# Optimization experiments

Hardware: AMD Instinct MI355X
Metric: run time of the kernel (lower is better)

Reference implementation:

```python
import jax, jax.numpy as jnp
import numpy as np

B, E, D, NH, NP = 4, 32, 1024, 16, 4
LQ = E * E
DH = D // NH


def layer_norm(x, g, b, eps=1e-6):
    m = x.mean(-1, keepdims=True)
    v = ((x - m) ** 2).mean(-1, keepdims=True)
    return (x - m) / jnp.sqrt(v + eps) * g + b


def get_ref(H, W):
    # matches MSCrossAttnBlock.get_reference_points: centers normalized to [0,1], (x, y) order
    ys, xs = jnp.meshgrid((jnp.arange(H, dtype=jnp.float32) + 0.5) / H,
                          (jnp.arange(W, dtype=jnp.float32) + 0.5) / W, indexing='ij')
    return jnp.stack([xs.ravel(), ys.ravel()], -1)  # (H*W, 2)


def bilinear_sample(value_l, loc, H, W):
    # value_l: (N, nH, H*W, dh); loc: (N, Lq, nH, P, 2) normalized to [0,1]
    # replicates F.grid_sample(align_corners=False, padding_mode='zeros') with grid = 2*loc - 1
    N, Lq, nH, P, _ = loc.shape
    x = loc[..., 0] * W - 0.5
    y = loc[..., 1] * H - 0.5
    x0 = jnp.floor(x)
    y0 = jnp.floor(y)
    wx1 = x - x0
    wy1 = y - y0
    out = 0.0
    for dy, wy in ((0, 1.0 - wy1), (1, wy1)):
        for dx, wx in ((0, 1.0 - wx1), (1, wx1)):
            xi = x0 + dx
            yi = y0 + dy
            valid = (xi >= 0) & (xi < W) & (yi >= 0) & (yi < H)
            idx = (jnp.clip(yi, 0, H - 1) * W + jnp.clip(xi, 0, W - 1)).astype(jnp.int32)
            idx_t = idx.transpose(0, 2, 1, 3).reshape(N, nH, Lq * P)  # (N, nH, Lq*P)
            g = jnp.take_along_axis(value_l, idx_t[..., None], axis=2)  # (N, nH, Lq*P, dh)
            g = g.reshape(N, nH, Lq, P, -1).transpose(0, 2, 1, 3, 4)  # (N, Lq, nH, P, dh)
            w = (wx * wy) * valid.astype(value_l.dtype)
            out = out + g * w[..., None]
    return out


def msdeform(query, ref, inp, shapes, Wv, bv, Wo, bo, Wa, ba, Wp, bp):
    # MSDeformAttn forward (no padding mask)
    N, Lq, d = query.shape
    nL = len(shapes)
    value = (inp @ Wv.T + bv).reshape(N, -1, NH, DH).transpose(0, 2, 1, 3)  # (N, nH, Lin, dh)
    off = (query @ Wo.T + bo).reshape(N, Lq, NH, nL, NP, 2)
    attw = jax.nn.softmax((query @ Wa.T + ba).reshape(N, Lq, NH, nL * NP), axis=-1)
    attw = attw.reshape(N, Lq, NH, nL, NP)
    normalizer = jnp.array([[w, h] for (h, w) in shapes], dtype=query.dtype)  # (nL, 2) = [W, H]
    loc = ref[None, :, None, None, None, :] + off / normalizer[None, None, None, :, None, :]
    out = 0.0
    start = 0
    for l, (H, W) in enumerate(shapes):
        sampled = bilinear_sample(value[:, :, start:start + H * W], loc[:, :, :, l], H, W)
        out = out + (sampled * attw[:, :, :, l, :, None]).sum(3)  # (N, Lq, nH, dh)
        start += H * W
    return out.reshape(N, Lq, d) @ Wp.T + bp


def setup_inputs() -> dict:
    key = jax.random.key(0)
    ks = iter(jax.random.split(key, 64))
    def rnd(shape, scale):
        return jax.random.normal(next(ks), shape, dtype=jnp.float32) * scale
    inp = {}
    for i in range(4):
        inp[f'src{i}'] = rnd((B, LQ, D), 1.0)
    for nm in ('qn', 'fn', 'n1'):
        inp[nm + '_g'] = jnp.ones((D,), jnp.float32)
        inp[nm + '_b'] = jnp.zeros((D,), jnp.float32)
    inp['gamma1'] = rnd((D,), 0.1)
    inp['gamma2'] = rnd((D,), 0.1)
    ws = D ** -0.5
    for pre, nl in (('ca', 4), ('sa', 1)):
        inp[pre + '_vw'] = rnd((D, D), ws)
        inp[pre + '_vb'] = jnp.zeros((D,), jnp.float32)
        inp[pre + '_ow'] = rnd((NH * nl * NP * 2, D), ws)
        inp[pre + '_ob'] = rnd((NH * nl * NP * 2,), 0.1)
        inp[pre + '_aw'] = rnd((NH * nl * NP, D), ws)
        inp[pre + '_ab'] = jnp.zeros((NH * nl * NP,), jnp.float32)
        inp[pre + '_pw'] = rnd((D, D), ws)
        inp[pre + '_pb'] = jnp.zeros((D,), jnp.float32)
    return inp


def reference(src0, src1, src2, src3, qn_g, qn_b, fn_g, fn_b, n1_g, n1_b, gamma1, gamma2,
              ca_vw, ca_vb, ca_ow, ca_ob, ca_aw, ca_ab, ca_pw, ca_pb,
              sa_vw, sa_vb, sa_ow, sa_ob, sa_aw, sa_ab, sa_pw, sa_pb):
    shapes4 = [(E, E)] * 4
    feat = jnp.concatenate([src0, src1, src2, src3], axis=1)  # (B, 4*LQ, D)
    query = src3  # srcs[-1], pos embed is None
    ref = get_ref(E, E)  # (LQ, 2)
    attn = msdeform(layer_norm(query, qn_g, qn_b), ref, layer_norm(feat, fn_g, fn_b),
                    shapes4, ca_vw, ca_vb, ca_ow, ca_ob, ca_aw, ca_ab, ca_pw, ca_pb)
    attn1 = layer_norm(attn, n1_g, n1_b)
    attn2 = msdeform(attn1, ref, attn1, [(E, E)],
                     sa_vw, sa_vb, sa_ow, sa_ob, sa_aw, sa_ab, sa_pw, sa_pb)
    attn = attn + gamma2 * attn2
    return query + gamma1 * attn
```

## Files before the change

kernel.cpp:

```cpp
#include <hip/hip_runtime.h>


#define DEV __device__ __forceinline__

typedef float f32x4 __attribute__((ext_vector_type(4)));
typedef __bf16 bf16x8 __attribute__((ext_vector_type(8)));

DEV unsigned short f2bf(float f) {
  union { float f; unsigned u; } a; a.f = f;
  unsigned r = a.u + 0x7fffu + ((a.u >> 16) & 1u);
  return (unsigned short)(r >> 16);
}
DEV float bf2f(unsigned short h) {
  union { unsigned u; float f; } a; a.u = ((unsigned)h) << 16;
  return a.f;
}

struct CvtArgs {
  const float* src[8];
  unsigned short* dst;
  int off4[9];
};
struct LnArgs {
  const float* s[4];
  const float* fg; const float* fb; const float* qg; const float* qb;
  unsigned short* f_out; unsigned short* q_out;
};

DEV void ln_row_wave(const float* __restrict__ xr, const float* __restrict__ g,
                     const float* __restrict__ b,
                     unsigned short* __restrict__ op_row) {
  const int lane = threadIdx.x & 63;
  float4 v[4];
  float s = 0.f, s2 = 0.f;
  #pragma unroll
  for (int j = 0; j < 4; ++j) {
    v[j] = ((const float4*)xr)[lane + 64 * j];
    s  += v[j].x + v[j].y + v[j].z + v[j].w;
    s2 += v[j].x*v[j].x + v[j].y*v[j].y + v[j].z*v[j].z + v[j].w*v[j].w;
  }
  #pragma unroll
  for (int o = 32; o; o >>= 1) { s += __shfl_xor(s, o); s2 += __shfl_xor(s2, o); }
  const float mean = s * (1.f / 1024.f);
  const float rstd = rsqrtf(s2 * (1.f / 1024.f) - mean * mean + 1e-6f);
  #pragma unroll
  for (int j = 0; j < 4; ++j) {
    float4 gg = ((const float4*)g)[lane + 64 * j];
    float4 bb = ((const float4*)b)[lane + 64 * j];
    ushort4 r;
    r.x = f2bf((v[j].x - mean) * rstd * gg.x + bb.x);
    r.y = f2bf((v[j].y - mean) * rstd * gg.y + bb.y);
    r.z = f2bf((v[j].z - mean) * rstd * gg.z + bb.z);
    r.w = f2bf((v[j].w - mean) * rstd * gg.w + bb.w);
    ((ushort4*)op_row)[lane + 64 * j] = r;
  }
}

__global__ __launch_bounds__(256) void prep_kernel(CvtArgs a, LnArgs L) {
  if (blockIdx.x < 5056) {
    int i = blockIdx.x * 256 + threadIdx.x;
    int seg = 0;
    #pragma unroll
    for (int s = 1; s < 8; ++s) seg += (i >= a.off4[s]) ? 1 : 0;
    const float4 v = ((const float4*)a.src[seg])[i - a.off4[seg]];
    unsigned short* o = a.dst + (size_t)i * 4;
    o[0] = f2bf(v.x); o[1] = f2bf(v.y); o[2] = f2bf(v.z); o[3] = f2bf(v.w);
  } else {
    int row = (blockIdx.x - 5056) * 4 + (threadIdx.x >> 6);
    if (row < 16384) {
      int l = row >> 12, inner = row & 4095;
      int orow = (inner >> 10) * 4096 + l * 1024 + (inner & 1023);
      ln_row_wave(L.s[l] + (size_t)inner * 1024, L.fg, L.fb,
                  L.f_out + (size_t)orow * 1024);
    } else {
      int inner = row - 16384;
      ln_row_wave(L.s[3] + (size_t)inner * 1024, L.qg, L.qb,
                  L.q_out + (size_t)inner * 1024);
    }
  }
}

__global__ __launch_bounds__(256) void ln_wave_kernel(
    const float* __restrict__ x, const float* __restrict__ g,
    const float* __restrict__ b, unsigned short* __restrict__ out) {
  int row = blockIdx.x * 4 + (threadIdx.x >> 6);
  ln_row_wave(x + (size_t)row * 1024, g, b, out + (size_t)row * 1024);
}

struct GemmP {
  const unsigned short* A; const unsigned short* W;
  void* C; void* C1; void* C2;
  const float* b0; const float* b1; const float* b2;
  const float* src3; const float* g1; const float* g2; const float* attnp;
  int M, N, K, tilesM;
};

template <int BM, int BN, int EPI>
DEV void gemm_body(const GemmP& P, int id, unsigned short* sA,
                   unsigned short* sB) {
  constexpr int WMT = BM / 2, WNT = BN / 2;
  constexpr int MF = WMT / 16, NF = WNT / 16;
  constexpr int PA = BM / 64, PB = BN / 64;
  const int tid = threadIdx.x;
  const int wave = tid >> 6, lane = tid & 63;
  const int wm = (wave & 1) * WMT, wn = (wave >> 1) * WNT;
  const int m0 = (id % P.tilesM) * BM;
  const int n0 = (id / P.tilesM) * BN;
  const int lq = lane >> 4, lm = lane & 15;
  const int r16 = lane >> 2;
  const int cst = lane & 3;
  const int csrc = cst ^ ((r16 >> 1) & 3);
  const int aslot = lq ^ ((lm >> 1) & 3);

  f32x4 acc[MF][NF] = {};
  bf16x8 ald[2][PA], bld[2][PB];

  #pragma unroll 1
  for (int k0 = 0; k0 < P.K; k0 += 64) {
    #pragma unroll
    for (int s = 0; s < 2; ++s) {
      #pragma unroll
      for (int p = 0; p < PA; ++p) {
        int grow = m0 + (wave + 4 * p) * 16 + r16;
        ald[s][p] = *(const bf16x8*)(P.A + (size_t)grow * P.K + k0 + s * 32 + csrc * 8);
      }
      #pragma unroll
      for (int p = 0; p < PB; ++p) {
        int grow = min(n0 + (wave + 4 * p) * 16 + r16, P.N - 1);
        bld[s][p] = *(const bf16x8*)(P.W + (size_t)grow * P.K + k0 + s * 32 + csrc * 8);
      }
    }
    __syncthreads();
    #pragma unroll
    for (int s = 0; s < 2; ++s) {
      #pragma unroll
      for (int p = 0; p < PA; ++p)
        *(bf16x8*)(sA + s * BM * 32 + (wave + 4 * p) * 512 + (r16 * 4 + cst) * 8) = ald[s][p];
      #pragma unroll
      for (int p = 0; p < PB; ++p)
        *(bf16x8*)(sB + s * BN * 32 + (wave + 4 * p) * 512 + (r16 * 4 + cst) * 8) = bld[s][p];
    }
    __syncthreads();
    #pragma unroll
    for (int s = 0; s < 2; ++s) {
      bf16x8 af[MF], bfr[NF];
      #pragma unroll
      for (int mi = 0; mi < MF; ++mi)
        af[mi] = *(const bf16x8*)(sA + s * BM * 32 + ((wm >> 4) + mi) * 512 + lm * 32 + aslot * 8);
      #pragma unroll
      for (int ni = 0; ni < NF; ++ni)
        bfr[ni] = *(const bf16x8*)(sB + s * BN * 32 + ((wn >> 4) + ni) * 512 + lm * 32 + aslot * 8);
      #pragma unroll
      for (int mi = 0; mi < MF; ++mi)
        #pragma unroll
        for (int ni = 0; ni < NF; ++ni)
          acc[mi][ni] = __builtin_amdgcn_mfma_f32_16x16x32_bf16(
              af[mi], bfr[ni], acc[mi][ni], 0, 0, 0);
    }
  }

  #pragma unroll
  for (int mi = 0; mi < MF; ++mi) {
    #pragma unroll
    for (int ni = 0; ni < NF; ++ni) {
      const int col = n0 + wn + ni * 16 + lm;
      #pragma unroll
      for (int r2 = 0; r2 < 4; ++r2) {
        const int row = m0 + wm + mi * 16 + lq * 4 + r2;
        float v = acc[mi][ni][r2];
        if constexpr (EPI == 0) {
          ((float*)P.C)[(size_t)row * 1024 + col] = v + P.b0[col];
        } else if constexpr (EPI == 1) {
          ((unsigned short*)P.C)[(size_t)row * 1024 + col] = f2bf(v + P.b0[col]);
        } else if constexpr (EPI == 2) {
          if (col < 512)
            ((float*)P.C)[(size_t)row * 512 + col] = v + P.b0[col];
          else
            ((float*)P.C1)[(size_t)row * 256 + col - 512] = v + P.b1[col - 512];
        } else if constexpr (EPI == 3) {
          if (col < 1024)
            ((unsigned short*)P.C)[(size_t)row * 1024 + col] = f2bf(v + P.b0[col]);
          else if (col < 1152)
            ((float*)P.C1)[(size_t)row * 128 + col - 1024] = v + P.b1[col - 1024];
          else if (col < 1216)
            ((float*)P.C2)[(size_t)row * 64 + col - 1152] = v + P.b2[col - 1152];
        } else {
          size_t i = (size_t)row * 1024 + col;
          float vv = v + P.b0[col];
          ((float*)P.C)[i] = P.src3[i] + P.g1[col] * (P.attnp[i] + P.g2[col] * vv);
        }
      }
    }
  }
}

template <int BM, int BN, int EPI>
__global__ __launch_bounds__(256) void gemm_v3(GemmP P) {
  extern __shared__ __align__(16) unsigned short smem[];
  gemm_body<BM, BN, EPI>(P, blockIdx.x, smem, smem + BM * 64);
}

template <int BM, int BN>
__global__ __launch_bounds__(256) void gemm_dual(GemmP Pv, GemmP Po, int split) {
  extern __shared__ __align__(16) unsigned short smem[];
  if ((int)blockIdx.x < split)
    gemm_body<BM, BN, 1>(Pv, blockIdx.x, smem, smem + BM * 64);
  else
    gemm_body<BM, BN, 2>(Po, blockIdx.x - split, smem, smem + BM * 64);
}

template <int NLEV>
__global__ __launch_bounds__(256) void ms_sample_fused(
    const unsigned short* __restrict__ value, const float* __restrict__ off,
    const float* __restrict__ logits, unsigned short* __restrict__ out) {
  const int nq = blockIdx.x;
  const int wave = threadIdx.x >> 6, lane = threadIdx.x & 63;
  const int h = (wave << 2) + (lane >> 4);
  const int c = (lane & 15) << 2;
  const int q = nq & 1023, n = nq >> 10;
  const float* offp = off + ((size_t)nq * 16 + h) * (NLEV * 8);
  const float* lgp  = logits + ((size_t)nq * 16 + h) * (NLEV * 4);

  float lg[NLEV * 4];
  #pragma unroll
  for (int i = 0; i < NLEV; ++i) {
    float4 v = ((const float4*)lgp)[i];
    lg[4*i] = v.x; lg[4*i+1] = v.y; lg[4*i+2] = v.z; lg[4*i+3] = v.w;
  }
  float mx = lg[0];
  #pragma unroll
  for (int i = 1; i < NLEV * 4; ++i) mx = fmaxf(mx, lg[i]);
  float ssum = 0.f;
  #pragma unroll
  for (int i = 0; i < NLEV * 4; ++i) { lg[i] = __expf(lg[i] - mx); ssum += lg[i]; }
  const float inv = 1.f / ssum;

  const float fqx = (float)(q & 31), fqy = (float)(q >> 5);
  float a0 = 0.f, a1 = 0.f, a2 = 0.f, a3 = 0.f;

  #pragma unroll
  for (int l = 0; l < NLEV; ++l) {
    const unsigned short* vl =
        value + ((size_t)(n * NLEV + l) << 20) + h * 64 + c;
    #pragma unroll
    for (int p = 0; p < 4; ++p) {
      float2 o2 = ((const float2*)offp)[l * 4 + p];
      float aw = lg[l * 4 + p] * inv;
      float xx = fqx + o2.x, yy = fqy + o2.y;
      float xf = floorf(xx), yf = floorf(yy);
      float fx = xx - xf, fy = yy - yf;
      int ix = (int)xf, iy = (int)yf;
      int ix1 = ix + 1, iy1 = iy + 1;
      float vx0 = ((unsigned)ix  < 32u) ? 1.f : 0.f;
      float vx1 = ((unsigned)ix1 < 32u) ? 1.f : 0.f;
      float vy0 = ((unsigned)iy  < 32u) ? 1.f : 0.f;
      float vy1 = ((unsigned)iy1 < 32u) ? 1.f : 0.f;
      int cx0 = min(max(ix, 0), 31), cx1 = min(max(ix1, 0), 31);
      int cy0 = min(max(iy, 0), 31), cy1 = min(max(iy1, 0), 31);
      float w00 = (1.f - fx) * (1.f - fy) * vx0 * vy0 * aw;
      float w01 = fx * (1.f - fy) * vx1 * vy0 * aw;
      float w10 = (1.f - fx) * fy * vx0 * vy1 * aw;
      float w11 = fx * fy * vx1 * vy1 * aw;
      ushort4 u00 = *(const ushort4*)(vl + ((size_t)(cy0 * 32 + cx0) << 10));
      ushort4 u01 = *(const ushort4*)(vl + ((size_t)(cy0 * 32 + cx1) << 10));
      ushort4 u10 = *(const ushort4*)(vl + ((size_t)(cy1 * 32 + cx0) << 10));
      ushort4 u11 = *(const ushort4*)(vl + ((size_t)(cy1 * 32 + cx1) << 10));
      a0 += w00 * bf2f(u00.x) + w01 * bf2f(u01.x) + w10 * bf2f(u10.x) + w11 * bf2f(u11.x);
      a1 += w00 * bf2f(u00.y) + w01 * bf2f(u01.y) + w10 * bf2f(u10.y) + w11 * bf2f(u11.y);
      a2 += w00 * bf2f(u00.z) + w01 * bf2f(u01.z) + w10 * bf2f(u10.z) + w11 * bf2f(u11.z);
      a3 += w00 * bf2f(u00.w) + w01 * bf2f(u01.w) + w10 * bf2f(u10.w) + w11 * bf2f(u11.w);
    }
  }
  ushort4 r;
  r.x = f2bf(a0); r.y = f2bf(a1); r.z = f2bf(a2); r.w = f2bf(a3);
  *(ushort4*)(out + ((size_t)nq * 16 + h) * 64 + c) = r;
}

extern "C" void kernel_launch(void* const* d_in, const int* in_sizes, int n_in,
                              void* d_out, int out_size, void* d_ws,
                              size_t ws_size, hipStream_t stream) {
  (void)in_sizes; (void)n_in; (void)out_size; (void)ws_size;
  const float* src[4] = {(const float*)d_in[0], (const float*)d_in[1],
                         (const float*)d_in[2], (const float*)d_in[3]};
  const float* qn_g = (const float*)d_in[4];
  const float* qn_b = (const float*)d_in[5];
  const float* fn_g = (const float*)d_in[6];
  const float* fn_b = (const float*)d_in[7];
  const float* n1_g = (const float*)d_in[8];
  const float* n1_b = (const float*)d_in[9];
  const float* gamma1 = (const float*)d_in[10];
  const float* gamma2 = (const float*)d_in[11];
  const float* ca_vw = (const float*)d_in[12];
  const float* ca_vb = (const float*)d_in[13];
  const float* ca_ow = (const float*)d_in[14];
  const float* ca_ob = (const float*)d_in[15];
  const float* ca_aw = (const float*)d_in[16];
  const float* ca_ab = (const float*)d_in[17];
  const float* ca_pw = (const float*)d_in[18];
  const float* ca_pb = (const float*)d_in[19];
  const float* sa_vw = (const float*)d_in[20];
  const float* sa_vb = (const float*)d_in[21];
  const float* sa_ow = (const float*)d_in[22];
  const float* sa_ob = (const float*)d_in[23];
  const float* sa_aw = (const float*)d_in[24];
  const float* sa_ab = (const float*)d_in[25];
  const float* sa_pw = (const float*)d_in[26];
  const float* sa_pb = (const float*)d_in[27];

  char* wsp = (char*)d_ws;
  size_t off = 0;
  auto alloc = [&](size_t bytes) {
    char* r = wsp + off;
    off = (off + bytes + 255) & ~(size_t)255;
    return r;
  };
  const size_t MB = 1024 * 1024;
  unsigned short* w_ca_vw = (unsigned short*)alloc(1024 * 1024 * 2);
  unsigned short* w_ca_ow = (unsigned short*)alloc(512 * 1024 * 2);
  unsigned short* w_ca_aw = (unsigned short*)alloc(256 * 1024 * 2);
  unsigned short* w_ca_pw = (unsigned short*)alloc(1024 * 1024 * 2);
  unsigned short* w_sa_vw = (unsigned short*)alloc(1024 * 1024 * 2);
  unsigned short* w_sa_ow = (unsigned short*)alloc(128 * 1024 * 2);
  unsigned short* w_sa_aw = (unsigned short*)alloc(64 * 1024 * 2);
  unsigned short* w_sa_pw = (unsigned short*)alloc(1024 * 1024 * 2);
  (void)w_ca_aw; (void)w_sa_ow; (void)w_sa_aw;
  char* R1 = alloc(32 * MB);
  char* R2 = alloc(32 * MB);
  char* R3 = alloc(8 * MB);
  char* R4 = alloc(8 * MB);
  char* R5 = alloc(4 * MB);

  unsigned short* f_ln    = (unsigned short*)R1;
  float*          attn    = (float*)R1;
  unsigned short* attn1   = (unsigned short*)(R1 + 16 * MB);
  unsigned short* samp_sa = (unsigned short*)(R1 + 24 * MB);
  unsigned short* val_ca  = (unsigned short*)R2;
  unsigned short* val_sa  = (unsigned short*)R2;
  unsigned short* q_ln    = (unsigned short*)R3;
  unsigned short* samp_ca = (unsigned short*)R3;
  float*          off_ca  = (float*)R4;
  float*          off_sa  = (float*)R4;
  float*          attw_sa = (float*)(R4 + 4 * MB);
  float*          attw_ca = (float*)R5;

  CvtArgs ca;
  ca.src[0] = ca_vw; ca.src[1] = ca_ow; ca.src[2] = ca_aw; ca.src[3] = ca_pw;
  ca.src[4] = sa_vw; ca.src[5] = sa_ow; ca.src[6] = sa_aw; ca.src[7] = sa_pw;
  ca.dst = w_ca_vw;
  const int sizes4[8] = {262144, 131072, 65536, 262144, 262144, 32768, 16384, 262144};
  ca.off4[0] = 0;
  for (int i = 0; i < 8; ++i) ca.off4[i + 1] = ca.off4[i] + sizes4[i];
  LnArgs la;
  la.s[0] = src[0]; la.s[1] = src[1]; la.s[2] = src[2]; la.s[3] = src[3];
  la.fg = fn_g; la.fb = fn_b; la.qg = qn_g; la.qb = qn_b;
  la.f_out = f_ln; la.q_out = q_ln;
  prep_kernel<<<10176, 256, 0, stream>>>(ca, la);

  auto mkP = [](const unsigned short* A, const unsigned short* W, void* C,
                const float* b0, int M, int N, int K, int tilesM) {
    GemmP p{}; p.A = A; p.W = W; p.C = C; p.b0 = b0;
    p.M = M; p.N = N; p.K = K; p.tilesM = tilesM;
    return p;
  };

  {
    GemmP pv = mkP(f_ln, w_ca_vw, val_ca, ca_vb, 16384, 1024, 1024, 128);
    GemmP po = mkP(q_ln, w_ca_ow, off_ca, ca_ob, 4096, 768, 1024, 32);
    po.C1 = attw_ca; po.b1 = ca_ab;
    gemm_dual<128, 128><<<1024 + 192, 256, 32768, stream>>>(pv, po, 1024);
  }

  ms_sample_fused<4><<<4096, 256, 0, stream>>>(val_ca, off_ca, attw_ca, samp_ca);
  gemm_v3<64, 128, 0><<<64 * 8, 256, (64 + 128) * 64 * 2, stream>>>(
      mkP(samp_ca, w_ca_pw, attn, ca_pb, 4096, 1024, 1024, 64));

  ln_wave_kernel<<<1024, 256, 0, stream>>>(attn, n1_g, n1_b, attn1);
  {
    GemmP p = mkP(attn1, w_sa_vw, val_sa, sa_vb, 4096, 1216, 1024, 64);
    p.C1 = off_sa; p.b1 = sa_ob; p.C2 = attw_sa; p.b2 = sa_ab;
    gemm_v3<64, 128, 3><<<64 * 10, 256, (64 + 128) * 64 * 2, stream>>>(p);
  }
  ms_sample_fused<1><<<4096, 256, 0, stream>>>(val_sa, off_sa, attw_sa, samp_sa);
  {
    GemmP p = mkP(samp_sa, w_sa_pw, d_out, sa_pb, 4096, 1024, 1024, 64);
    p.src3 = src[3]; p.g1 = gamma1; p.g2 = gamma2; p.attnp = attn;
    gemm_v3<64, 128, 4><<<64 * 8, 256, (64 + 128) * 64 * 2, stream>>>(p);
  }
}
```

Before: 370.9 us.

## Store attn as bf16, widen sampler loads, share LN stats for src3

The intermediate attn tensor is now stored as bf16 instead of fp32, and the following layer norm and final epilogue are adapted to read bf16. This halves that tensor's write and read traffic but adds bf16 rounding to the residual path. The deformable sampler now gathers 8 channels per lane with 16-byte loads, and its block-to-query mapping is remapped across 2048 blocks. The prep kernel computes src3 layer-norm statistics once and applies both the feature and query norms from them, which removes one extra pass over src3.

```diff
diff --git a/kernel.cpp b/kernel.cpp
--- a/kernel.cpp
+++ b/kernel.cpp
@@ -5,6 +5,7 @@
 
 typedef float f32x4 __attribute__((ext_vector_type(4)));
 typedef __bf16 bf16x8 __attribute__((ext_vector_type(8)));
+typedef unsigned short u16x8 __attribute__((ext_vector_type(8)));
 
 DEV unsigned short f2bf(float f) {
   union { float f; unsigned u; } a; a.f = f;
@@ -27,11 +28,9 @@
   unsigned short* f_out; unsigned short* q_out;
 };
 
-DEV void ln_row_wave(const float* __restrict__ xr, const float* __restrict__ g,
-                     const float* __restrict__ b,
-                     unsigned short* __restrict__ op_row) {
+DEV void ln_stats(const float* __restrict__ xr, float4 (&v)[4], float& mean,
+                  float& rstd) {
   const int lane = threadIdx.x & 63;
-  float4 v[4];
   float s = 0.f, s2 = 0.f;
   #pragma unroll
   for (int j = 0; j < 4; ++j) {
@@ -41,8 +40,14 @@
   }
   #pragma unroll
   for (int o = 32; o; o >>= 1) { s += __shfl_xor(s, o); s2 += __shfl_xor(s2, o); }
-  const float mean = s * (1.f / 1024.f);
-  const float rstd = rsqrtf(s2 * (1.f / 1024.f) - mean * mean + 1e-6f);
+  mean = s * (1.f / 1024.f);
+  rstd = rsqrtf(s2 * (1.f / 1024.f) - mean * mean + 1e-6f);
+}
+
+DEV void ln_apply(const float4 (&v)[4], float mean, float rstd,
+                  const float* __restrict__ g, const float* __restrict__ b,
+                  unsigned short* __restrict__ op_row) {
+  const int lane = threadIdx.x & 63;
   #pragma unroll
   for (int j = 0; j < 4; ++j) {
     float4 gg = ((const float4*)g)[lane + 64 * j];
@@ -67,31 +72,55 @@
     o[0] = f2bf(v.x); o[1] = f2bf(v.y); o[2] = f2bf(v.z); o[3] = f2bf(v.w);
   } else {
     int row = (blockIdx.x - 5056) * 4 + (threadIdx.x >> 6);
-    if (row < 16384) {
-      int l = row >> 12, inner = row & 4095;
-      int orow = (inner >> 10) * 4096 + l * 1024 + (inner & 1023);
-      ln_row_wave(L.s[l] + (size_t)inner * 1024, L.fg, L.fb,
-                  L.f_out + (size_t)orow * 1024);
-    } else {
-      int inner = row - 16384;
-      ln_row_wave(L.s[3] + (size_t)inner * 1024, L.qg, L.qb,
-                  L.q_out + (size_t)inner * 1024);
-    }
-  }
-}
-
-__global__ __launch_bounds__(256) void ln_wave_kernel(
-    const float* __restrict__ x, const float* __restrict__ g,
+    int l = row >> 12, inner = row & 4095;
+    int orow = (inner >> 10) * 4096 + l * 1024 + (inner & 1023);
+    float4 v[4]; float mean, rstd;
+    ln_stats(L.s[l] + (size_t)inner * 1024, v, mean, rstd);
+    ln_apply(v, mean, rstd, L.fg, L.fb, L.f_out + (size_t)orow * 1024);
+    if (l == 3)
+      ln_apply(v, mean, rstd, L.qg, L.qb, L.q_out + (size_t)inner * 1024);
+  }
+}
+
+__global__ __launch_bounds__(256) void ln_wave_bf16(
+    const unsigned short* __restrict__ x, const float* __restrict__ g,
     const float* __restrict__ b, unsigned short* __restrict__ out) {
   int row = blockIdx.x * 4 + (threadIdx.x >> 6);
-  ln_row_wave(x + (size_t)row * 1024, g, b, out + (size_t)row * 1024);
+  const int lane = threadIdx.x & 63;
+  const unsigned short* xr = x + (size_t)row * 1024;
+  float e[16];
+  float s = 0.f, s2 = 0.f;
+  #pragma unroll
+  for (int j = 0; j < 2; ++j) {
+    u16x8 u = ((const u16x8*)xr)[lane + 64 * j];
+    #pragma unroll
+    for (int k = 0; k < 8; ++k) {
+      float f = bf2f(u[k]);
+      e[j * 8 + k] = f; s += f; s2 += f * f;
+    }
+  }
+  #pragma unroll
+  for (int o = 32; o; o >>= 1) { s += __shfl_xor(s, o); s2 += __shfl_xor(s2, o); }
+  const float mean = s * (1.f / 1024.f);
+  const float rstd = rsqrtf(s2 * (1.f / 1024.f) - mean * mean + 1e-6f);
+  #pragma unroll
+  for (int j = 0; j < 2; ++j) {
+    u16x8 r;
+    #pragma unroll
+    for (int k = 0; k < 8; ++k) {
+      int idx = (lane + 64 * j) * 8 + k;
+      r[k] = f2bf((e[j * 8 + k] - mean) * rstd * g[idx] + b[idx]);
+    }
+    ((u16x8*)(out + (size_t)row * 1024))[lane + 64 * j] = r;
+  }
 }
 
 struct GemmP {
   const unsigned short* A; const unsigned short* W;
   void* C; void* C1; void* C2;
   const float* b0; const float* b1; const float* b2;
-  const float* src3; const float* g1; const float* g2; const float* attnp;
+  const float* src3; const float* g1; const float* g2;
+  const unsigned short* attnp;
   int M, N, K, tilesM;
 };
 
@@ -168,9 +197,7 @@
       for (int r2 = 0; r2 < 4; ++r2) {
         const int row = m0 + wm + mi * 16 + lq * 4 + r2;
         float v = acc[mi][ni][r2];
-        if constexpr (EPI == 0) {
-          ((float*)P.C)[(size_t)row * 1024 + col] = v + P.b0[col];
-        } else if constexpr (EPI == 1) {
+        if constexpr (EPI == 1) {
           ((unsigned short*)P.C)[(size_t)row * 1024 + col] = f2bf(v + P.b0[col]);
         } else if constexpr (EPI == 2) {
           if (col < 512)
@@ -187,7 +214,8 @@
         } else {
           size_t i = (size_t)row * 1024 + col;
           float vv = v + P.b0[col];
-          ((float*)P.C)[i] = P.src3[i] + P.g1[col] * (P.attnp[i] + P.g2[col] * vv);
+          float at = bf2f(P.attnp[i]);
+          ((float*)P.C)[i] = P.src3[i] + P.g1[col] * (at + P.g2[col] * vv);
         }
       }
     }
@@ -210,14 +238,16 @@
 }
 
 template <int NLEV>
-__global__ __launch_bounds__(256) void ms_sample_fused(
+__global__ __launch_bounds__(256) void ms_sample_v2(
     const unsigned short* __restrict__ value, const float* __restrict__ off,
     const float* __restrict__ logits, unsigned short* __restrict__ out) {
-  const int nq = blockIdx.x;
+  const int b = blockIdx.x;
   const int wave = threadIdx.x >> 6, lane = threadIdx.x & 63;
-  const int h = (wave << 2) + (lane >> 4);
-  const int c = (lane & 15) << 2;
-  const int q = nq & 1023, n = nq >> 10;
+  const int n = (b & 7) >> 1;
+  const int q = ((b & 1) << 9) + ((b >> 3) << 1) + (wave >> 1);
+  const int nq = (n << 10) + q;
+  const int h = ((wave & 1) << 3) + (lane >> 3);
+  const int c = (lane & 7) << 3;
   const float* offp = off + ((size_t)nq * 16 + h) * (NLEV * 8);
   const float* lgp  = logits + ((size_t)nq * 16 + h) * (NLEV * 4);
 
@@ -236,7 +266,7 @@
   const float inv = 1.f / ssum;
 
   const float fqx = (float)(q & 31), fqy = (float)(q >> 5);
-  float a0 = 0.f, a1 = 0.f, a2 = 0.f, a3 = 0.f;
+  float a[8] = {};
 
   #pragma unroll
   for (int l = 0; l < NLEV; ++l) {
@@ -261,19 +291,20 @@
       float w01 = fx * (1.f - fy) * vx1 * vy0 * aw;
       float w10 = (1.f - fx) * fy * vx0 * vy1 * aw;
       float w11 = fx * fy * vx1 * vy1 * aw;
-      ushort4 u00 = *(const ushort4*)(vl + ((size_t)(cy0 * 32 + cx0) << 10));
-      ushort4 u01 = *(const ushort4*)(vl + ((size_t)(cy0 * 32 + cx1) << 10));
-      ushort4 u10 = *(const ushort4*)(vl + ((size_t)(cy1 * 32 + cx0) << 10));
-      ushort4 u11 = *(const ushort4*)(vl + ((size_t)(cy1 * 32 + cx1) << 10));
-      a0 += w00 * bf2f(u00.x) + w01 * bf2f(u01.x) + w10 * bf2f(u10.x) + w11 * bf2f(u11.x);
-      a1 += w00 * bf2f(u00.y) + w01 * bf2f(u01.y) + w10 * bf2f(u10.y) + w11 * bf2f(u11.y);
-      a2 += w00 * bf2f(u00.z) + w01 * bf2f(u01.z) + w10 * bf2f(u10.z) + w11 * bf2f(u11.z);
-      a3 += w00 * bf2f(u00.w) + w01 * bf2f(u01.w) + w10 * bf2f(u10.w) + w11 * bf2f(u11.w);
-    }
-  }
-  ushort4 r;
-  r.x = f2bf(a0); r.y = f2bf(a1); r.z = f2bf(a2); r.w = f2bf(a3);
-  *(ushort4*)(out + ((size_t)nq * 16 + h) * 64 + c) = r;
+      u16x8 u00 = *(const u16x8*)(vl + ((size_t)(cy0 * 32 + cx0) << 10));
+      u16x8 u01 = *(const u16x8*)(vl + ((size_t)(cy0 * 32 + cx1) << 10));
+      u16x8 u10 = *(const u16x8*)(vl + ((size_t)(cy1 * 32 + cx0) << 10));
+      u16x8 u11 = *(const u16x8*)(vl + ((size_t)(cy1 * 32 + cx1) << 10));
+      #pragma unroll
+      for (int k = 0; k < 8; ++k)
+        a[k] += w00 * bf2f(u00[k]) + w01 * bf2f(u01[k]) +
+                w10 * bf2f(u10[k]) + w11 * bf2f(u11[k]);
+    }
+  }
+  u16x8 r;
+  #pragma unroll
+  for (int k = 0; k < 8; ++k) r[k] = f2bf(a[k]);
+  *(u16x8*)(out + ((size_t)nq * 16 + h) * 64 + c) = r;
 }
 
 extern "C" void kernel_launch(void* const* d_in, const int* in_sizes, int n_in,
@@ -331,9 +362,9 @@
   char* R5 = alloc(4 * MB);
 
   unsigned short* f_ln    = (unsigned short*)R1;
-  float*          attn    = (float*)R1;
-  unsigned short* attn1   = (unsigned short*)(R1 + 16 * MB);
-  unsigned short* samp_sa = (unsigned short*)(R1 + 24 * MB);
+  unsigned short* attn    = (unsigned short*)R1;
+  unsigned short* attn1   = (unsigned short*)(R1 + 8 * MB);
+  unsigned short* samp_sa = (unsigned short*)(R1 + 16 * MB);
   unsigned short* val_ca  = (unsigned short*)R2;
   unsigned short* val_sa  = (unsigned short*)R2;
   unsigned short* q_ln    = (unsigned short*)R3;
@@ -354,7 +385,7 @@
   la.s[0] = src[0]; la.s[1] = src[1]; la.s[2] = src[2]; la.s[3] = src[3];
   la.fg = fn_g; la.fb = fn_b; la.qg = qn_g; la.qb = qn_b;
   la.f_out = f_ln; la.q_out = q_ln;
-  prep_kernel<<<10176, 256, 0, stream>>>(ca, la);
+  prep_kernel<<<5056 + 4096, 256, 0, stream>>>(ca, la);
 
   auto mkP = [](const unsigned short* A, const unsigned short* W, void* C,
                 const float* b0, int M, int N, int K, int tilesM) {
@@ -370,17 +401,17 @@
     gemm_dual<128, 128><<<1024 + 192, 256, 32768, stream>>>(pv, po, 1024);
   }
 
-  ms_sample_fused<4><<<4096, 256, 0, stream>>>(val_ca, off_ca, attw_ca, samp_ca);
-  gemm_v3<64, 128, 0><<<64 * 8, 256, (64 + 128) * 64 * 2, stream>>>(
+  ms_sample_v2<4><<<2048, 256, 0, stream>>>(val_ca, off_ca, attw_ca, samp_ca);
+  gemm_v3<64, 128, 1><<<64 * 8, 256, (64 + 128) * 64 * 2, stream>>>(
       mkP(samp_ca, w_ca_pw, attn, ca_pb, 4096, 1024, 1024, 64));
 
-  ln_wave_kernel<<<1024, 256, 0, stream>>>(attn, n1_g, n1_b, attn1);
+  ln_wave_bf16<<<1024, 256, 0, stream>>>(attn, n1_g, n1_b, attn1);
   {
     GemmP p = mkP(attn1, w_sa_vw, val_sa, sa_vb, 4096, 1216, 1024, 64);
     p.C1 = off_sa; p.b1 = sa_ob; p.C2 = attw_sa; p.b2 = sa_ab;
     gemm_v3<64, 128, 3><<<64 * 10, 256, (64 + 128) * 64 * 2, stream>>>(p);
   }
-  ms_sample_fused<1><<<4096, 256, 0, stream>>>(val_sa, off_sa, attw_sa, samp_sa);
+  ms_sample_v2<1><<<2048, 256, 0, stream>>>(val_sa, off_sa, attw_sa, samp_sa);
   {
     GemmP p = mkP(samp_sa, w_sa_pw, d_out, sa_pb, 4096, 1024, 1024, 64);
     p.src3 = src[3]; p.g1 = gamma1; p.g2 = gamma2; p.attnp = attn;
```

Measured after the change: 368.7 us. No clear change (-0.6%).
